# Performance work log

Measured on AMD Instinct MI355X. Metric: run time of the kernel, lower is better.

Reference implementation:

```python
import jax, jax.numpy as jnp
import numpy as np
from jax import lax

# Static problem sizes (see shape_source)
B, C, N = 32, 512, 64
SENTS_PER_VIDEO = 4
TARGETS_PER_SENT = 2
S = B * SENTS_PER_VIDEO          # 128 sentences
M = S * TARGETS_PER_SENT         # 256 target moments
P = N * (N + 1) // 2             # 2080 valid proposals (upper-tri mask2d)
T_TEMP = 0.1
MARGIN = 0.0
NEG_IOU = 0.5
K_TOP = 1                        # pos_topk
WEIGHT = 1.0


def setup_inputs() -> dict:
    key = jax.random.key(0)
    k1, k2, k3, k4 = jax.random.split(key, 4)
    return {
        "video_feats": jax.random.normal(k1, (B, C, N, N), jnp.float32),
        "sents_feats": jax.random.normal(k2, (S, C), jnp.float32),
        "num_sentences": jnp.full((B,), SENTS_PER_VIDEO, jnp.int32),
        "num_targets": jnp.full((S,), TARGETS_PER_SENT, jnp.int32),
        "iou2d": jax.random.uniform(k3, (S, N, N), jnp.float32),
        "iou2ds": jax.random.uniform(k4, (M, N, N), jnp.float32),
        "mask2d": jnp.triu(jnp.ones((N, N), bool)),
        "epoch": 0,  # < start_DNS_epoch -> DNS branch skipped
    }


def _log_cross_entropy(pos_scores, all_scores, neg_mask, t, m):
    # Faithful to LogCrossEntropy.forward
    pos_exp = jnp.exp((pos_scores - m) / t)
    neg_exp_sum = jnp.sum(jnp.exp(all_scores / t) * neg_mask, axis=-1)
    loss = -((pos_scores - m) / t - jnp.log(pos_exp + neg_exp_sum))
    return jnp.mean(loss)


def _l2_normalize(x, axis=-1, eps=1e-12):
    n = jnp.linalg.norm(x, axis=axis, keepdims=True)
    return x / jnp.maximum(n, eps)


def reference(video_feats, sents_feats, num_sentences, num_targets,
              iou2d, iou2ds, mask2d, epoch):
    # Compact valid proposals (P is static: upper-triangular mask2d)
    idx = jnp.nonzero(mask2d.reshape(-1), size=P)[0]              # (P,)
    v = video_feats.reshape(B, C, N * N)[:, :, idx]               # (B,C,P)
    v = jnp.transpose(v, (0, 2, 1))                               # (B,P,C)
    iou2d_f = iou2d.reshape(S, N * N)[:, idx]                     # (S,P)
    iou2ds_f = iou2ds.reshape(M, N * N)[:, idx]                   # (M,P)

    v = _l2_normalize(v)
    sents = _l2_normalize(sents_feats)

    scatter_s2v = jnp.repeat(jnp.arange(B), num_sentences, total_repeat_length=S)
    scatter_m2s = jnp.repeat(jnp.arange(S), num_targets, total_repeat_length=M)
    scatter_m2v = scatter_s2v[scatter_m2s]

    # top-K proposals per target moment by IoU
    topk_idx = lax.top_k(iou2ds_f, K_TOP)[1]                      # (M,K)
    topk_v = jnp.take_along_axis(v[scatter_m2v], topk_idx[:, :, None], axis=1)  # (M,K,C)

    # inter-video loss
    inter_video_pos = jnp.einsum('mkc,mc->mk', topk_v, sents[scatter_m2s])  # (M,K)
    inter_video_all = jnp.einsum('mkc,sc->mks', topk_v, sents)              # (M,K,S)
    inter_video_neg_mask = (~jnp.eye(S, dtype=bool))[scatter_m2s][:, None, :]  # (M,1,S)
    loss_inter_video = _log_cross_entropy(
        inter_video_pos, inter_video_all, inter_video_neg_mask, T_TEMP, MARGIN)

    # inter-query loss
    inter_query_pos = inter_video_pos                              # (M,K)
    inter_query_all = (sents @ v.reshape(B * P, C).T)[:, None, :]  # (S,1,B*P)
    # pos_mask: block-diagonal per video, refined by IoU > neg_iou inside own block
    onehot = jnp.eye(B, dtype=bool)[scatter_s2v]                   # (S,B)
    pos_mask = (onehot[:, :, None] & (iou2d_f > NEG_IOU)[:, None, :]).reshape(S, B * P)
    inter_query_neg_mask = (~pos_mask)[:, None, :]                 # (S,1,B*P)
    loss_inter_query = _log_cross_entropy(
        inter_query_pos, inter_query_all[scatter_m2s],
        inter_query_neg_mask[scatter_m2s], T_TEMP, MARGIN)

    total = (loss_inter_video + loss_inter_query) * WEIGHT
    return total, loss_inter_video, loss_inter_query
```

## Files before the change

kernel.cpp:

```cpp
#include <hip/hip_runtime.h>
#include <cstdint>

#define BB 32
#define CC 512
#define NSQ 4096
#define SS 128
#define MM 256
#define PP 2080
#define JJ (BB*PP)

#define WS_SN     0
#define WS_IDX    262144
#define WS_TOPIDX 270464
#define WS_TV     271488
#define WS_IV     795776
#define WS_NEGQ   926848

__global__ void k_prep(const float* __restrict__ sents, float* __restrict__ sn,
                       int* __restrict__ idx, float* __restrict__ negq) {
    const int blk = blockIdx.x, t = threadIdx.x;
    if (blk < 128) {
        __shared__ float red[256];
        const float* row = sents + (size_t)blk * CC;
        float x0 = row[t], x1 = row[t + 256];
        red[t] = x0 * x0 + x1 * x1;
        __syncthreads();
        for (int off = 128; off > 0; off >>= 1) {
            if (t < off) red[t] += red[t + off];
            __syncthreads();
        }
        float rn = 1.0f / fmaxf(sqrtf(red[0]), 1e-12f);
        sn[(size_t)blk * CC + t]       = x0 * rn;
        sn[(size_t)blk * CC + t + 256] = x1 * rn;
    } else if (blk < 144) {
        int i = (blk - 128) * 256 + t;
        int r = i >> 6, c = i & 63;
        if (c >= r) {
            int p = r * 64 - (r * (r - 1)) / 2 + (c - r);
            idx[p] = i;
        }
    } else {
        if (t < 128) negq[t] = 0.0f;
    }
}

__global__ void k_argmax(const float* __restrict__ iou2ds, const int* __restrict__ idx,
                         int* __restrict__ topidx) {
    const int m = blockIdx.x, t = threadIdx.x;
    __shared__ float sv[256];
    __shared__ int   si[256];
    float best = -1e30f; int bi = PP;
    const float* row = iou2ds + (size_t)m * NSQ;
    for (int p = t; p < PP; p += 256) {
        float v = row[idx[p]];
        if (v > best || (v == best && p < bi)) { best = v; bi = p; }
    }
    sv[t] = best; si[t] = bi;
    __syncthreads();
    for (int off = 128; off > 0; off >>= 1) {
        if (t < off) {
            float v2 = sv[t + off]; int i2 = si[t + off];
            if (v2 > sv[t] || (v2 == sv[t] && i2 < si[t])) { sv[t] = v2; si[t] = i2; }
        }
        __syncthreads();
    }
    if (t == 0) topidx[m] = si[0];
}

__global__ void k_topkv(const float* __restrict__ video, const int* __restrict__ idx,
                        const int* __restrict__ topidx, float* __restrict__ tv) {
    const int m = blockIdx.x, t = threadIdx.x;
    __shared__ float red[256];
    const int b = m >> 3;
    const int flat = idx[topidx[m]];
    const float* base = video + (size_t)b * CC * NSQ + flat;
    float x0 = base[(size_t)t * NSQ];
    float x1 = base[(size_t)(t + 256) * NSQ];
    red[t] = x0 * x0 + x1 * x1;
    __syncthreads();
    for (int off = 128; off > 0; off >>= 1) {
        if (t < off) red[t] += red[t + off];
        __syncthreads();
    }
    float rn = 1.0f / fmaxf(sqrtf(red[0]), 1e-12f);
    tv[(size_t)m * CC + t]       = x0 * rn;
    tv[(size_t)m * CC + t + 256] = x1 * rn;
}

__global__ void k_ivall(const float* __restrict__ tv, const float* __restrict__ sn,
                        float* __restrict__ iv) {
    const int m = blockIdx.x, t = threadIdx.x;
    __shared__ float4 tvs[128];
    const float4* tv4 = (const float4*)(tv + (size_t)m * CC);
    tvs[t] = tv4[t];
    __syncthreads();
    const float4* sn4 = (const float4*)(sn + (size_t)t * CC);
    float acc = 0.f;
#pragma unroll 4
    for (int c = 0; c < 128; c++) {
        float4 a = tvs[c]; float4 b = sn4[c];
        acc += a.x * b.x + a.y * b.y + a.z * b.z + a.w * b.w;
    }
    iv[(size_t)m * SS + t] = acc;
}

__global__ __launch_bounds__(256)
void k_big(const float* __restrict__ video, const float* __restrict__ sn,
           const float* __restrict__ iou2d, const int* __restrict__ idx,
           float* __restrict__ negq) {
    __shared__ float sA[16][132];
    __shared__ float vB[16][128];
    __shared__ float colrn[128];
    __shared__ int   colb[128], colflat[128];
    __shared__ float sq2[2][128];
    __shared__ float red[128][16];

    const int t  = threadIdx.x;
    const int tx = t & 15, ty = t >> 4;
    const int j0 = blockIdx.x * 128;

    if (t < 128) {
        int col = j0 + t;
        int b = col / PP;
        int p = col - b * PP;
        colb[t] = b;
        colflat[t] = idx[p];
    }

    const int jj = t & 127;
    const int kh = t >> 7;
    {
    }
    int colL = j0 + jj;
    int bL = colL / PP;
    int pL = colL - bL * PP;
    int flatL = idx[pL];
    const float* vptr = video + (size_t)bL * (CC * NSQ) + flatL + (size_t)kh * 8 * NSQ;

    float acc[8][8];
#pragma unroll
    for (int i = 0; i < 8; i++)
#pragma unroll
        for (int j = 0; j < 8; j++) acc[i][j] = 0.f;

    float sqa = 0.f;

    for (int k0 = 0; k0 < CC; k0 += 16) {
        __syncthreads();
        {
            int lin = t;
#pragma unroll
            for (int it = 0; it < 2; it++) {
                int s = lin >> 2, q = lin & 3;
                float4 w = *(const float4*)(sn + (size_t)s * CC + k0 + q * 4);
                sA[q * 4 + 0][s] = w.x;
                sA[q * 4 + 1][s] = w.y;
                sA[q * 4 + 2][s] = w.z;
                sA[q * 4 + 3][s] = w.w;
                lin += 256;
            }
        }
        {
            const float* vp = vptr + (size_t)k0 * NSQ;
#pragma unroll
            for (int i = 0; i < 8; i++) {
                float x = vp[(size_t)i * NSQ];
                sqa += x * x;
                vB[kh * 8 + i][jj] = x;
            }
        }
        __syncthreads();
#pragma unroll
        for (int kk = 0; kk < 16; kk++) {
            float4 a0 = *(const float4*)&sA[kk][ty * 8];
            float4 a1 = *(const float4*)&sA[kk][ty * 8 + 4];
            float4 b0 = *(const float4*)&vB[kk][tx * 8];
            float4 b1 = *(const float4*)&vB[kk][tx * 8 + 4];
            float av[8] = {a0.x, a0.y, a0.z, a0.w, a1.x, a1.y, a1.z, a1.w};
            float bv[8] = {b0.x, b0.y, b0.z, b0.w, b1.x, b1.y, b1.z, b1.w};
#pragma unroll
            for (int i = 0; i < 8; i++)
#pragma unroll
                for (int j = 0; j < 8; j++)
                    acc[i][j] += av[i] * bv[j];
        }
    }

    sq2[kh][jj] = sqa;
    __syncthreads();
    if (t < 128) {
        float s2 = sq2[0][t] + sq2[1][t];
        colrn[t] = 1.0f / fmaxf(sqrtf(s2), 1e-12f);
    }
    __syncthreads();

    float rowsum[8];
#pragma unroll
    for (int i = 0; i < 8; i++) rowsum[i] = 0.f;

#pragma unroll
    for (int j = 0; j < 8; j++) {
        int cidx = tx * 8 + j;
        float rn = colrn[cidx];
        int b = colb[cidx];
        int flat = colflat[cidx];
#pragma unroll
        for (int i = 0; i < 8; i++) {
            int s = ty * 8 + i;
            float sc = acc[i][j] * rn;
            float e = expf(sc * 10.0f);
            if ((s >> 2) == b) {
                if (iou2d[(size_t)s * NSQ + flat] > 0.5f) e = 0.f;
            }
            rowsum[i] += e;
        }
    }
#pragma unroll
    for (int i = 0; i < 8; i++) red[ty * 8 + i][tx] = rowsum[i];
    __syncthreads();
    if (t < 128) {
        float tot = 0.f;
#pragma unroll
        for (int x = 0; x < 16; x++) tot += red[t][x];
        atomicAdd(&negq[t], tot);
    }
}

__global__ void k_final(const float* __restrict__ iv, const float* __restrict__ negq,
                        float* __restrict__ out) {
    const int t = threadIdx.x;
    __shared__ float rv[256], rq[256];
    const float* row = iv + (size_t)t * SS;
    const int ms = t >> 1;
    float pos = row[ms];
    float nv = 0.f;
    for (int s = 0; s < SS; s++) {
        float e = expf(row[s] * 10.0f);
        if (s == ms) e = 0.f;
        nv += e;
    }
    float pe = expf(pos * 10.0f);
    float lv = logf(pe + nv) - pos * 10.0f;
    float lq = logf(pe + negq[ms]) - pos * 10.0f;
    rv[t] = lv; rq[t] = lq;
    __syncthreads();
    for (int off = 128; off > 0; off >>= 1) {
        if (t < off) { rv[t] += rv[t + off]; rq[t] += rq[t + off]; }
        __syncthreads();
    }
    if (t == 0) {
        float liv = rv[0] / 256.f, liq = rq[0] / 256.f;
        out[0] = liv + liq;
        out[1] = liv;
        out[2] = liq;
    }
}

extern "C" void kernel_launch(void* const* d_in, const int* in_sizes, int n_in,
                              void* d_out, int out_size, void* d_ws, size_t ws_size,
                              hipStream_t stream) {
    const float* video  = (const float*)d_in[0];
    const float* sents  = (const float*)d_in[1];
    const float* iou2d  = (const float*)d_in[4];
    const float* iou2ds = (const float*)d_in[5];
    float* out = (float*)d_out;

    char* ws = (char*)d_ws;
    float* sn     = (float*)(ws + WS_SN);
    int*   idx    = (int*)  (ws + WS_IDX);
    int*   topidx = (int*)  (ws + WS_TOPIDX);
    float* tv     = (float*)(ws + WS_TV);
    float* iv     = (float*)(ws + WS_IV);
    float* negq   = (float*)(ws + WS_NEGQ);

    k_prep  <<<145, 256, 0, stream>>>(sents, sn, idx, negq);
    k_argmax<<<MM,  256, 0, stream>>>(iou2ds, idx, topidx);
    k_topkv <<<MM,  256, 0, stream>>>(video, idx, topidx, tv);
    k_ivall <<<MM,  128, 0, stream>>>(tv, sn, iv);
    k_big   <<<JJ / 128, 256, 0, stream>>>(video, sn, iou2d, idx, negq);
    k_final <<<1,   256, 0, stream>>>(iv, negq, out);
}
```

Measured before the change: 489.4 us.

## Move big similarity GEMM to bf16 MFMA and fuse argmax/topk/iv kernels

The main sentence-by-proposal GEMM now converts the normalized sentences and gathered video features to bf16 and uses 16x16x32 bf16 MFMA instructions with a 64-wide K tile, replacing the fp32 FMA outer-product loop. The argmax, top-k gather and inter-video dot-product kernels are merged into one kernel to cut launches and intermediate buffers. This aims to remove the FP32 compute bound of the big kernel. It trades away precision, since the scores pass through exp(10x), and the video gather stays a strided fp32 load.

```diff
diff --git a/kernel.cpp b/kernel.cpp
--- a/kernel.cpp
+++ b/kernel.cpp
@@ -10,13 +10,22 @@
 #define JJ (BB*PP)
 
 #define WS_SN     0
-#define WS_IDX    262144
-#define WS_TOPIDX 270464
-#define WS_TV     271488
-#define WS_IV     795776
-#define WS_NEGQ   926848
+#define WS_SNB    262144
+#define WS_IDX    393216
+#define WS_IV     401536
+#define WS_NEGQ   532608
+
+typedef short bf16x8 __attribute__((ext_vector_type(8)));
+typedef float f32x4  __attribute__((ext_vector_type(4)));
+
+__device__ __forceinline__ unsigned short f2bf(float x) {
+    unsigned int u = __float_as_uint(x);
+    unsigned int r = (u + 0x7fffu + ((u >> 16) & 1u)) >> 16;
+    return (unsigned short)r;
+}
 
 __global__ void k_prep(const float* __restrict__ sents, float* __restrict__ sn,
+                       unsigned short* __restrict__ snb,
                        int* __restrict__ idx, float* __restrict__ negq) {
     const int blk = blockIdx.x, t = threadIdx.x;
     if (blk < 128) {
@@ -30,8 +39,11 @@
             __syncthreads();
         }
         float rn = 1.0f / fmaxf(sqrtf(red[0]), 1e-12f);
-        sn[(size_t)blk * CC + t]       = x0 * rn;
-        sn[(size_t)blk * CC + t + 256] = x1 * rn;
+        float y0 = x0 * rn, y1 = x1 * rn;
+        sn[(size_t)blk * CC + t]        = y0;
+        sn[(size_t)blk * CC + t + 256]  = y1;
+        snb[(size_t)blk * CC + t]       = f2bf(y0);
+        snb[(size_t)blk * CC + t + 256] = f2bf(y1);
     } else if (blk < 144) {
         int i = (blk - 128) * 256 + t;
         int r = i >> 6, c = i & 63;
@@ -44,35 +56,35 @@
     }
 }
 
-__global__ void k_argmax(const float* __restrict__ iou2ds, const int* __restrict__ idx,
-                         int* __restrict__ topidx) {
+__global__ void k_fused(const float* __restrict__ video, const float* __restrict__ sn,
+                        const float* __restrict__ iou2ds, const int* __restrict__ idx,
+                        float* __restrict__ iv) {
     const int m = blockIdx.x, t = threadIdx.x;
     __shared__ float sv[256];
     __shared__ int   si[256];
-    float best = -1e30f; int bi = PP;
-    const float* row = iou2ds + (size_t)m * NSQ;
-    for (int p = t; p < PP; p += 256) {
-        float v = row[idx[p]];
-        if (v > best || (v == best && p < bi)) { best = v; bi = p; }
-    }
-    sv[t] = best; si[t] = bi;
-    __syncthreads();
-    for (int off = 128; off > 0; off >>= 1) {
-        if (t < off) {
-            float v2 = sv[t + off]; int i2 = si[t + off];
-            if (v2 > sv[t] || (v2 == sv[t] && i2 < si[t])) { sv[t] = v2; si[t] = i2; }
-        }
-        __syncthreads();
-    }
-    if (t == 0) topidx[m] = si[0];
-}
-
-__global__ void k_topkv(const float* __restrict__ video, const int* __restrict__ idx,
-                        const int* __restrict__ topidx, float* __restrict__ tv) {
-    const int m = blockIdx.x, t = threadIdx.x;
+    __shared__ float tvs[512];
     __shared__ float red[256];
+
+    {
+        float best = -1e30f; int bi = 1 << 30;
+        const float* row = iou2ds + (size_t)m * NSQ;
+        for (int p = t; p < PP; p += 256) {
+            float v = row[idx[p]];
+            if (v > best || (v == best && p < bi)) { best = v; bi = p; }
+        }
+        sv[t] = best; si[t] = bi;
+        __syncthreads();
+        for (int off = 128; off > 0; off >>= 1) {
+            if (t < off) {
+                float v2 = sv[t + off]; int i2 = si[t + off];
+                if (v2 > sv[t] || (v2 == sv[t] && i2 < si[t])) { sv[t] = v2; si[t] = i2; }
+            }
+            __syncthreads();
+        }
+    }
+    const int flat = idx[si[0]];
     const int b = m >> 3;
-    const int flat = idx[topidx[m]];
+
     const float* base = video + (size_t)b * CC * NSQ + flat;
     float x0 = base[(size_t)t * NSQ];
     float x1 = base[(size_t)(t + 256) * NSQ];
@@ -83,140 +95,138 @@
         __syncthreads();
     }
     float rn = 1.0f / fmaxf(sqrtf(red[0]), 1e-12f);
-    tv[(size_t)m * CC + t]       = x0 * rn;
-    tv[(size_t)m * CC + t + 256] = x1 * rn;
-}
-
-__global__ void k_ivall(const float* __restrict__ tv, const float* __restrict__ sn,
-                        float* __restrict__ iv) {
-    const int m = blockIdx.x, t = threadIdx.x;
-    __shared__ float4 tvs[128];
-    const float4* tv4 = (const float4*)(tv + (size_t)m * CC);
-    tvs[t] = tv4[t];
-    __syncthreads();
-    const float4* sn4 = (const float4*)(sn + (size_t)t * CC);
+    tvs[t] = x0 * rn;
+    tvs[t + 256] = x1 * rn;
+    __syncthreads();
+
+    const int s = t & 127, h = t >> 7;
+    const float4* a4 = (const float4*)(tvs + h * 256);
+    const float4* b4 = (const float4*)(sn + (size_t)s * CC + h * 256);
     float acc = 0.f;
-#pragma unroll 4
-    for (int c = 0; c < 128; c++) {
-        float4 a = tvs[c]; float4 b = sn4[c];
-        acc += a.x * b.x + a.y * b.y + a.z * b.z + a.w * b.w;
-    }
-    iv[(size_t)m * SS + t] = acc;
-}
+#pragma unroll 8
+    for (int c = 0; c < 64; c++) {
+        float4 a = a4[c], bb = b4[c];
+        acc += a.x * bb.x + a.y * bb.y + a.z * bb.z + a.w * bb.w;
+    }
+    __syncthreads();
+    red[t] = acc;
+    __syncthreads();
+    if (t < 128) iv[(size_t)m * SS + t] = red[t] + red[t + 128];
+}
+
+#define BK 64
+#define LDK 72
 
 __global__ __launch_bounds__(256)
-void k_big(const float* __restrict__ video, const float* __restrict__ sn,
+void k_big(const float* __restrict__ video, const unsigned short* __restrict__ snb,
            const float* __restrict__ iou2d, const int* __restrict__ idx,
            float* __restrict__ negq) {
-    __shared__ float sA[16][132];
-    __shared__ float vB[16][128];
+    __shared__ unsigned short sA[128 * LDK];
+    __shared__ unsigned short vB[128 * LDK];
+    __shared__ int   colb[128], colflat[128];
     __shared__ float colrn[128];
-    __shared__ int   colb[128], colflat[128];
-    __shared__ float sq2[2][128];
-    __shared__ float red[128][16];
-
-    const int t  = threadIdx.x;
-    const int tx = t & 15, ty = t >> 4;
-    const int j0 = blockIdx.x * 128;
+    __shared__ float sqpart[256];
+    __shared__ float red[128][17];
+
+    const int t    = threadIdx.x;
+    const int w    = t >> 6;
+    const int lane = t & 63;
+    const int q    = lane >> 4;
+    const int l15  = lane & 15;
+    const int j0   = blockIdx.x * 128;
 
     if (t < 128) {
         int col = j0 + t;
         int b = col / PP;
-        int p = col - b * PP;
         colb[t] = b;
-        colflat[t] = idx[p];
+        colflat[t] = idx[col - b * PP];
     }
 
     const int jj = t & 127;
     const int kh = t >> 7;
-    {
-    }
     int colL = j0 + jj;
     int bL = colL / PP;
-    int pL = colL - bL * PP;
-    int flatL = idx[pL];
-    const float* vptr = video + (size_t)bL * (CC * NSQ) + flatL + (size_t)kh * 8 * NSQ;
-
-    float acc[8][8];
-#pragma unroll
-    for (int i = 0; i < 8; i++)
-#pragma unroll
-        for (int j = 0; j < 8; j++) acc[i][j] = 0.f;
+    int flatL = idx[colL - bL * PP];
+    const float* vbase = video + (size_t)bL * (CC * NSQ) + flatL;
+
+    f32x4 acc[2][8];
+#pragma unroll
+    for (int i = 0; i < 2; i++)
+#pragma unroll
+        for (int j = 0; j < 8; j++) acc[i][j] = (f32x4){0.f, 0.f, 0.f, 0.f};
 
     float sqa = 0.f;
 
-    for (int k0 = 0; k0 < CC; k0 += 16) {
-        __syncthreads();
+    for (int k0 = 0; k0 < CC; k0 += BK) {
+        __syncthreads();
+#pragma unroll
+        for (int it = 0; it < 4; it++) {
+            int lin = t + it * 256;
+            int row = lin >> 3, kc = (lin & 7) * 8;
+            bf16x8 v = *(const bf16x8*)(snb + (size_t)row * CC + k0 + kc);
+            *(bf16x8*)(sA + row * LDK + kc) = v;
+        }
         {
-            int lin = t;
-#pragma unroll
-            for (int it = 0; it < 2; it++) {
-                int s = lin >> 2, q = lin & 3;
-                float4 w = *(const float4*)(sn + (size_t)s * CC + k0 + q * 4);
-                sA[q * 4 + 0][s] = w.x;
-                sA[q * 4 + 1][s] = w.y;
-                sA[q * 4 + 2][s] = w.z;
-                sA[q * 4 + 3][s] = w.w;
-                lin += 256;
-            }
-        }
-        {
-            const float* vp = vptr + (size_t)k0 * NSQ;
-#pragma unroll
-            for (int i = 0; i < 8; i++) {
-                float x = vp[(size_t)i * NSQ];
-                sqa += x * x;
-                vB[kh * 8 + i][jj] = x;
-            }
-        }
-        __syncthreads();
-#pragma unroll
-        for (int kk = 0; kk < 16; kk++) {
-            float4 a0 = *(const float4*)&sA[kk][ty * 8];
-            float4 a1 = *(const float4*)&sA[kk][ty * 8 + 4];
-            float4 b0 = *(const float4*)&vB[kk][tx * 8];
-            float4 b1 = *(const float4*)&vB[kk][tx * 8 + 4];
-            float av[8] = {a0.x, a0.y, a0.z, a0.w, a1.x, a1.y, a1.z, a1.w};
-            float bv[8] = {b0.x, b0.y, b0.z, b0.w, b1.x, b1.y, b1.z, b1.w};
-#pragma unroll
-            for (int i = 0; i < 8; i++)
-#pragma unroll
-                for (int j = 0; j < 8; j++)
-                    acc[i][j] += av[i] * bv[j];
-        }
-    }
-
-    sq2[kh][jj] = sqa;
-    __syncthreads();
-    if (t < 128) {
-        float s2 = sq2[0][t] + sq2[1][t];
-        colrn[t] = 1.0f / fmaxf(sqrtf(s2), 1e-12f);
-    }
-    __syncthreads();
-
-    float rowsum[8];
-#pragma unroll
-    for (int i = 0; i < 8; i++) rowsum[i] = 0.f;
-
-#pragma unroll
-    for (int j = 0; j < 8; j++) {
-        int cidx = tx * 8 + j;
-        float rn = colrn[cidx];
-        int b = colb[cidx];
-        int flat = colflat[cidx];
-#pragma unroll
-        for (int i = 0; i < 8; i++) {
-            int s = ty * 8 + i;
-            float sc = acc[i][j] * rn;
-            float e = expf(sc * 10.0f);
-            if ((s >> 2) == b) {
-                if (iou2d[(size_t)s * NSQ + flat] > 0.5f) e = 0.f;
-            }
-            rowsum[i] += e;
-        }
-    }
-#pragma unroll
-    for (int i = 0; i < 8; i++) red[ty * 8 + i][tx] = rowsum[i];
+            const float* vp = vbase + (size_t)(k0 + kh * 32) * NSQ;
+#pragma unroll
+            for (int g = 0; g < 4; g++) {
+                unsigned short buf[8];
+#pragma unroll
+                for (int i = 0; i < 8; i++) {
+                    float x = vp[(size_t)(g * 8 + i) * NSQ];
+                    sqa += x * x;
+                    buf[i] = f2bf(x);
+                }
+                *(bf16x8*)(vB + jj * LDK + kh * 32 + g * 8) = *(bf16x8*)buf;
+            }
+        }
+        __syncthreads();
+#pragma unroll
+        for (int ks = 0; ks < BK; ks += 32) {
+            bf16x8 a[2], bfr[8];
+#pragma unroll
+            for (int rt = 0; rt < 2; rt++) {
+                int row = w * 32 + rt * 16 + l15;
+                a[rt] = *(const bf16x8*)(sA + row * LDK + ks + q * 8);
+            }
+#pragma unroll
+            for (int ct = 0; ct < 8; ct++) {
+                int col = ct * 16 + l15;
+                bfr[ct] = *(const bf16x8*)(vB + col * LDK + ks + q * 8);
+            }
+#pragma unroll
+            for (int rt = 0; rt < 2; rt++)
+#pragma unroll
+                for (int ct = 0; ct < 8; ct++)
+                    acc[rt][ct] = __builtin_amdgcn_mfma_f32_16x16x32_bf16(
+                        a[rt], bfr[ct], acc[rt][ct], 0, 0, 0);
+        }
+    }
+
+    sqpart[t] = sqa;
+    __syncthreads();
+    if (t < 128) colrn[t] = 1.0f / fmaxf(sqrtf(sqpart[t] + sqpart[t + 128]), 1e-12f);
+    __syncthreads();
+
+#pragma unroll
+    for (int rt = 0; rt < 2; rt++) {
+#pragma unroll
+        for (int r = 0; r < 4; r++) {
+            int s = w * 32 + rt * 16 + q * 4 + r;
+            float rowsum = 0.f;
+#pragma unroll
+            for (int ct = 0; ct < 8; ct++) {
+                int c = ct * 16 + l15;
+                float sc = acc[rt][ct][r] * colrn[c];
+                float e = expf(sc * 10.0f);
+                if ((s >> 2) == colb[c]) {
+                    if (iou2d[(size_t)s * NSQ + colflat[c]] > 0.5f) e = 0.f;
+                }
+                rowsum += e;
+            }
+            red[s][l15] = rowsum;
+        }
+    }
     __syncthreads();
     if (t < 128) {
         float tot = 0.f;
@@ -266,17 +276,14 @@
     float* out = (float*)d_out;
 
     char* ws = (char*)d_ws;
-    float* sn     = (float*)(ws + WS_SN);
-    int*   idx    = (int*)  (ws + WS_IDX);
-    int*   topidx = (int*)  (ws + WS_TOPIDX);
-    float* tv     = (float*)(ws + WS_TV);
-    float* iv     = (float*)(ws + WS_IV);
-    float* negq   = (float*)(ws + WS_NEGQ);
-
-    k_prep  <<<145, 256, 0, stream>>>(sents, sn, idx, negq);
-    k_argmax<<<MM,  256, 0, stream>>>(iou2ds, idx, topidx);
-    k_topkv <<<MM,  256, 0, stream>>>(video, idx, topidx, tv);
-    k_ivall <<<MM,  128, 0, stream>>>(tv, sn, iv);
-    k_big   <<<JJ / 128, 256, 0, stream>>>(video, sn, iou2d, idx, negq);
-    k_final <<<1,   256, 0, stream>>>(iv, negq, out);
-}
+    float*          sn   = (float*)(ws + WS_SN);
+    unsigned short* snb  = (unsigned short*)(ws + WS_SNB);
+    int*            idx  = (int*)(ws + WS_IDX);
+    float*          iv   = (float*)(ws + WS_IV);
+    float*          negq = (float*)(ws + WS_NEGQ);
+
+    k_prep <<<145, 256, 0, stream>>>(sents, sn, snb, idx, negq);
+    k_big  <<<JJ / 128, 256, 0, stream>>>(video, snb, iou2d, idx, negq);
+    k_fused<<<MM,  256, 0, stream>>>(video, sn, iou2ds, idx, iv);
+    k_final<<<1,   256, 0, stream>>>(iv, negq, out);
+}
```

After: 439.0 us. -10.3%, faster.
